# Kernel tuning notes

Hardware: AMD Instinct MI355X
Metric: run time of the kernel (lower is better)

The kernel has to match this reference:

```python
import jax, jax.numpy as jnp
import numpy as np

_PADDING_NUM = -1


def setup_inputs() -> dict:
    key = jax.random.key(0)
    B, M, S, C = 4096, 64, 64, 4096  # batch, num_buckets, multiplex_count, channels
    x = jax.random.normal(key, (B, C), dtype=jnp.float32)
    # Full packing: each slot holds a unique object index (no padding).
    assignments = jnp.arange(B, dtype=jnp.int32).reshape(M, S)
    return {"x": x, "assignments": assignments}


def reference(x, assignments):
    """Mux (dispatch) then demux (combine) via precomputed one-hot transition matrices.

    x:           (B, C)  data-space tensor
    assignments: (M, S)  object index per (bucket, slot); _PADDING_NUM (-1) -> zero slot
    returns demuxed (B, C): data-space tensor recovered from multiplex space.
    """
    B = x.shape[0]
    valid = (assignments >= 0)  # (M, S)
    # Transition matrix: (M, S, B); padding slots map to all-zero rows.
    T = jax.nn.one_hot(jnp.where(valid, assignments, 0), B, dtype=x.dtype)
    T = T * valid[..., None].astype(x.dtype)
    # mux: place each valid object into its (bucket, slot); padding slots are zeros.
    muxed = jnp.einsum('msb,bc->msc', T, x)  # (M, S, C)
    # demux: gather slots back to data space in object-index order.
    demuxed = jnp.einsum('msb,msc->bc', T, muxed)  # (B, C)
    return demuxed
```

## Files before the change

### kernel.cpp

```cpp
#include <hip/hip_runtime.h>


#define BLOCK 256
#define C_VEC 1024
#define VPT 4
#define MS_VEC 1024
#define APT 4

__global__ __launch_bounds__(BLOCK) void mux_fused_kernel(
    const float4* __restrict__ x,
    const int4* __restrict__ a4,
    float4* __restrict__ out) {
    const int b = blockIdx.x;
    const int tid = threadIdx.x;

    const long base = (long)b * C_VEC;
    float4 v[VPT];
#pragma unroll
    for (int k = 0; k < VPT; ++k)
        v[k] = x[base + tid + BLOCK * k];

    int local = 0;
#pragma unroll
    for (int k = 0; k < APT; ++k) {
        int4 a = a4[tid + BLOCK * k];
        local += (a.x == b) + (a.y == b) + (a.z == b) + (a.w == b);
    }

#pragma unroll
    for (int off = 32; off > 0; off >>= 1)
        local += __shfl_down(local, off, 64);

    __shared__ int wave_sum[BLOCK / 64];
    __shared__ float s_scale;
    const int wave = tid >> 6;
    if ((tid & 63) == 0) wave_sum[wave] = local;
    __syncthreads();
    if (tid == 0)
        s_scale = (float)(wave_sum[0] + wave_sum[1] + wave_sum[2] + wave_sum[3]);
    __syncthreads();
    const float s = s_scale;

#pragma unroll
    for (int k = 0; k < VPT; ++k) {
        float4 w = v[k];
        w.x *= s; w.y *= s; w.z *= s; w.w *= s;
        out[base + tid + BLOCK * k] = w;
    }
}

extern "C" void kernel_launch(void* const* d_in, const int* in_sizes, int n_in,
                              void* d_out, int out_size, void* d_ws, size_t ws_size,
                              hipStream_t stream) {
    const float* x = (const float*)d_in[0];
    const int* assignments = (const int*)d_in[1];
    float* out = (float*)d_out;

    const int B = 4096;
    mux_fused_kernel<<<dim3(B), dim3(BLOCK), 0, stream>>>(
        (const float4*)x, (const int4*)assignments, (float4*)out);
}
```

Before: 110.1 us.

## Precompute per-row counts in a histogram kernel before scaling rows

Splits the fused kernel in two. A small kernel builds a histogram of assignment indices in LDS using shared atomics, with each block owning a range of 64 rows, and writes per-row scale factors to workspace. The scaling kernel then reads one float per row instead of every block rescanning the whole 16 KB assignment array and doing a block reduction. The cost is an extra kernel launch and a dependency through global workspace.

```diff
diff --git a/kernel.cpp b/kernel.cpp
--- a/kernel.cpp
+++ b/kernel.cpp
@@ -4,48 +4,54 @@
 #define BLOCK 256
 #define C_VEC 1024
 #define VPT 4
-#define MS_VEC 1024
+#define MS4 1024
 #define APT 4
+#define RANGE 64
+#define NROWS 4096
 
-__global__ __launch_bounds__(BLOCK) void mux_fused_kernel(
+__global__ __launch_bounds__(BLOCK) void count_kernel(
+    const int4* __restrict__ a4,
+    float* __restrict__ scale) {
+    __shared__ int bins[RANGE];
+    const int tid = threadIdx.x;
+    const int b0 = blockIdx.x * RANGE;
+
+    if (tid < RANGE) bins[tid] = 0;
+    __syncthreads();
+
+#pragma unroll
+    for (int k = 0; k < APT; ++k) {
+        const int4 a = a4[tid + BLOCK * k];
+        int d;
+        d = a.x - b0; if ((unsigned)d < RANGE) atomicAdd(&bins[d], 1);
+        d = a.y - b0; if ((unsigned)d < RANGE) atomicAdd(&bins[d], 1);
+        d = a.z - b0; if ((unsigned)d < RANGE) atomicAdd(&bins[d], 1);
+        d = a.w - b0; if ((unsigned)d < RANGE) atomicAdd(&bins[d], 1);
+    }
+    __syncthreads();
+
+    if (tid < RANGE) scale[b0 + tid] = (float)bins[tid];
+}
+
+__global__ __launch_bounds__(BLOCK) void scale_kernel(
     const float4* __restrict__ x,
-    const int4* __restrict__ a4,
+    const float* __restrict__ scale,
     float4* __restrict__ out) {
     const int b = blockIdx.x;
-    const int tid = threadIdx.x;
+    const long base = (long)b * C_VEC + threadIdx.x;
 
-    const long base = (long)b * C_VEC;
     float4 v[VPT];
 #pragma unroll
     for (int k = 0; k < VPT; ++k)
-        v[k] = x[base + tid + BLOCK * k];
+        v[k] = x[base + BLOCK * k];
 
-    int local = 0;
-#pragma unroll
-    for (int k = 0; k < APT; ++k) {
-        int4 a = a4[tid + BLOCK * k];
-        local += (a.x == b) + (a.y == b) + (a.z == b) + (a.w == b);
-    }
-
-#pragma unroll
-    for (int off = 32; off > 0; off >>= 1)
-        local += __shfl_down(local, off, 64);
-
-    __shared__ int wave_sum[BLOCK / 64];
-    __shared__ float s_scale;
-    const int wave = tid >> 6;
-    if ((tid & 63) == 0) wave_sum[wave] = local;
-    __syncthreads();
-    if (tid == 0)
-        s_scale = (float)(wave_sum[0] + wave_sum[1] + wave_sum[2] + wave_sum[3]);
-    __syncthreads();
-    const float s = s_scale;
+    const float s = scale[b];
 
 #pragma unroll
     for (int k = 0; k < VPT; ++k) {
         float4 w = v[k];
         w.x *= s; w.y *= s; w.z *= s; w.w *= s;
-        out[base + tid + BLOCK * k] = w;
+        out[base + BLOCK * k] = w;
     }
 }
 
@@ -55,8 +61,10 @@
     const float* x = (const float*)d_in[0];
     const int* assignments = (const int*)d_in[1];
     float* out = (float*)d_out;
+    float* scale = (float*)d_ws;
 
-    const int B = 4096;
-    mux_fused_kernel<<<dim3(B), dim3(BLOCK), 0, stream>>>(
-        (const float4*)x, (const int4*)assignments, (float4*)out);
+    count_kernel<<<dim3(NROWS / RANGE), dim3(BLOCK), 0, stream>>>(
+        (const int4*)assignments, scale);
+    scale_kernel<<<dim3(NROWS), dim3(BLOCK), 0, stream>>>(
+        (const float4*)x, scale, (float4*)out);
 }
```

After: 113.4 us. 1.03x slower.
